# Optimization experiments

Hardware: AMD Instinct MI355X
Metric: run time of the kernel (lower is better)

Reference implementation:

```python
import jax, jax.numpy as jnp
import numpy as np

B, T, P, N, U, L, K = 32, 12, 12, 512, 64, 2, 2
C = 2 * U  # combined_dim = input_dim(rnn_units) + rnn_units = 128


def setup_inputs():
    ks = jax.random.split(jax.random.key(0), 24)
    inp = {
        'x': jax.random.normal(ks[0], (B, T, N, 1), jnp.float32),
        'adj': jax.random.uniform(ks[1], (N, N), jnp.float32),
        'spatial_mask_1': 0.1 * jax.random.normal(ks[2], (N, N), jnp.float32),
        'spatial_mask_2': 0.1 * jax.random.normal(ks[3], (N, N), jnp.float32),
        'temporal_mask': 0.1 * jax.random.normal(ks[4], (T, N), jnp.float32),
        'fc_in_w': 0.1 * jax.random.normal(ks[5], (1, U), jnp.float32),
        'fc_in_b': jnp.zeros((U,), jnp.float32),
        'fc_out_w': 0.1 * jax.random.normal(ks[6], (U, 1), jnp.float32),
        'fc_out_b': jnp.zeros((1,), jnp.float32),
    }
    i = 7
    for pre in ('enc', 'dec'):
        for name, od in (('w_ru', 2 * U), ('w_c', U), ('w_ru2', 2 * U), ('w_c2', U)):
            inp[pre + '_' + name] = 0.08 * jax.random.normal(ks[i], (L, 2 * K, C, od), jnp.float32)
            i += 1
            inp[pre + '_' + name.replace('w', 'b')] = jnp.zeros((L, od), jnp.float32)
    return inp


def _supports(adj):
    # adj_hat = A + I; fwd = D_out^-1 A_hat ; bwd = D_in^-1 A_hat^T (inf -> 0)
    ah = adj + jnp.eye(adj.shape[0], dtype=adj.dtype)
    d_out = ah.sum(1)
    d_in = ah.sum(0)
    inv_out = jnp.where(d_out > 0, 1.0 / d_out, 0.0)
    inv_in = jnp.where(d_in > 0, 1.0 / d_in, 0.0)
    return inv_out[:, None] * ah, inv_in[:, None] * ah.T


def _dgc(x, sup, w, b):
    # x: [B,N,C]; sup: (fwd,bwd) each [N,N]; w: [2K,C,O]; b: [O]
    # The torch code expands x K times per support, so each k-slice of x_out is
    # identical: sum_k P_s @ w[k] == P_s @ w[sK:(s+1)K].sum(0). Same math, fused.
    pf = jnp.einsum('nm,bni->bmi', sup[0], x)
    pb = jnp.einsum('nm,bni->bmi', sup[1], x)
    return (jnp.einsum('bni,io->bno', pf, w[:K].sum(0))
            + jnp.einsum('bni,io->bno', pb, w[K:].sum(0)) + b)


def _cell(x, h, s1, s2, w_ru, b_ru, w_c, b_c, w_ru2, b_ru2, w_c2, b_c2):
    xh = jnp.concatenate([x, h], axis=-1)
    r1, u1 = jnp.split(jax.nn.sigmoid(_dgc(xh, s1, w_ru, b_ru)), 2, axis=-1)
    c1 = jnp.tanh(_dgc(jnp.concatenate([x, r1 * h], axis=-1), s1, w_c, b_c))
    r2, u2 = jnp.split(jax.nn.sigmoid(_dgc(xh, s2, w_ru2, b_ru2)), 2, axis=-1)
    c2 = jnp.tanh(_dgc(jnp.concatenate([x, r2 * h], axis=-1), s2, w_c2, b_c2))
    u = 0.5 * (u1 + u2)
    c = 0.5 * (c1 + c2)
    return (1.0 - u) * h + u * c


def _forward(x, adj, sm1, sm2, tm, fc_in_w, fc_in_b, fc_out_w, fc_out_b, enc, dec):
    x = x * (jnp.tanh(tm) + 1.0)[None, :, :, None]
    adj1 = adj * (jnp.tanh(0.5 * (sm1 + sm1.T)) + 1.0)
    adj2 = adj * (jnp.tanh(0.5 * (sm2 + sm2.T)) + 1.0)
    s1 = _supports(adj1)
    s2 = _supports(adj2)

    def run_layers(cells, inp, h):
        hs = []
        for i in range(L):
            hi = _cell(inp, h[i], s1, s2, *[p[i] for p in cells])
            hs.append(hi)
            inp = hi
        return jnp.stack(hs)

    def enc_step(h, xt):
        inp = xt @ fc_in_w + fc_in_b  # [B,N,U]
        return run_layers(enc, inp, h), None

    h0 = jnp.zeros((L, B, N, U), x.dtype)
    h, _ = jax.lax.scan(enc_step, h0, jnp.swapaxes(x, 0, 1))

    def dec_step(carry, _):
        h, go = carry
        inp = go @ fc_in_w + fc_in_b
        h = run_layers(dec, inp, h)
        out_t = h[-1] @ fc_out_w + fc_out_b  # [B,N,1]
        return (h, out_t), out_t

    _, outs = jax.lax.scan(dec_step, (h, jnp.zeros((B, N, 1), x.dtype)), None, length=P)
    return jnp.swapaxes(outs, 0, 1)[..., 0]  # [B,P,N]


def reference(x, adj, spatial_mask_1, spatial_mask_2, temporal_mask,
              fc_in_w, fc_in_b, fc_out_w, fc_out_b,
              enc_w_ru, enc_b_ru, enc_w_c, enc_b_c, enc_w_ru2, enc_b_ru2, enc_w_c2, enc_b_c2,
              dec_w_ru, dec_b_ru, dec_w_c, dec_b_c, dec_w_ru2, dec_b_ru2, dec_w_c2, dec_b_c2):
    enc = (enc_w_ru, enc_b_ru, enc_w_c, enc_b_c, enc_w_ru2, enc_b_ru2, enc_w_c2, enc_b_c2)
    dec = (dec_w_ru, dec_b_ru, dec_w_c, dec_b_c, dec_w_ru2, dec_b_ru2, dec_w_c2, dec_b_c2)
    return _forward(x, adj, spatial_mask_1, spatial_mask_2, temporal_mask,
                    fc_in_w, fc_in_b, fc_out_w, fc_out_b, enc, dec)
```

## Files before the change

kernel.cpp:

```cpp
#include <hip/hip_runtime.h>
#include <math.h>

#define NN 512
#define BB 32
#define UU 64
#define CC 128
#define TT 12
#define NP 12
#define RRR (NN*BB)

typedef _Float16 f16;
typedef f16 f16x8 __attribute__((ext_vector_type(8)));
typedef f16 f16x4 __attribute__((ext_vector_type(4)));
typedef float f32x4 __attribute__((ext_vector_type(4)));

__device__ __forceinline__ void gload16(const f16* g, f16* l) {
  __builtin_amdgcn_global_load_lds((const __attribute__((address_space(1))) void*)g,
                                   (__attribute__((address_space(3))) void*)l, 16, 0, 0);
}

static const size_t OFF_ST    = 0;
static const size_t OFF_AH    = OFF_ST   + (size_t)4*512*512;
static const size_t OFF_INVD  = OFF_AH   + (size_t)2*512*512;
static const size_t OFF_XH    = OFF_INVD + 2048;
static const size_t OFF_H     = OFF_XH   + (size_t)2*RRR*CC;
static const size_t OFF_RH    = OFF_H    + (size_t)2*RRR*UU;
static const size_t OFF_U     = OFF_RH   + (size_t)2*RRR*UU;
static const size_t OFF_CB    = OFF_U    + (size_t)2*RRR*UU;
static const size_t OFF_F16   = OFF_CB   + (size_t)2*RRR*UU;
static const size_t OFF_ST16A = OFF_F16;
static const size_t OFF_ST16B = OFF_ST16A + 524288;
static const size_t OFF_XHT1  = OFF_ST16B + 524288;
static const size_t OFF_XHT2  = OFF_XHT1  + 1048576;
static const size_t OFF_RHT1  = OFF_XHT2  + 1048576;
static const size_t OFF_RHT2  = OFF_RHT1  + 1048576;
static const size_t OFF_P1    = OFF_RHT2  + 1048576;
static const size_t OFF_P2    = OFF_P1    + 4194304;
static const size_t OFF_Q1    = OFF_P2    + 4194304;
static const size_t OFF_Q2    = OFF_Q1    + 2097152;
static const size_t OFF_WT1   = OFF_Q2    + 2097152;
static const size_t OFF_WT2   = OFF_WT1   + 196608;

__global__ void k_build_ah(const float* __restrict__ adj, const float* __restrict__ sm1,
                           const float* __restrict__ sm2, float* __restrict__ ah) {
  int a = blockIdx.y, i = blockIdx.x;
  const float* sm = a ? sm2 : sm1;
  for (int j = threadIdx.x; j < NN; j += blockDim.x) {
    float m = tanhf(0.5f * (sm[i*NN + j] + sm[j*NN + i])) + 1.0f;
    ah[((size_t)a*NN + i)*NN + j] = adj[i*NN + j] * m + ((i == j) ? 1.0f : 0.0f);
  }
}

__global__ void k_deg(const float* __restrict__ ah, float* __restrict__ invd) {
  int a = blockIdx.y, n = blockIdx.x;
  const float* A = ah + (size_t)a*NN*NN;
  __shared__ float sr[256], sc[256];
  int t = threadIdx.x;
  sr[t] = A[(size_t)n*NN + t] + A[(size_t)n*NN + t + 256];
  sc[t] = A[(size_t)t*NN + n] + A[(size_t)(t+256)*NN + n];
  __syncthreads();
  for (int s = 128; s > 0; s >>= 1) {
    if (t < s) { sr[t] += sr[t+s]; sc[t] += sc[t+s]; }
    __syncthreads();
  }
  if (t == 0) {
    float dr = sr[0], dc = sc[0];
    invd[(a*2 + 0)*NN + n] = dr > 0.f ? 1.f/dr : 0.f;
    invd[(a*2 + 1)*NN + n] = dc > 0.f ? 1.f/dc : 0.f;
  }
}

__global__ void k_st(const float* __restrict__ ah, const float* __restrict__ invd,
                     float* __restrict__ ST) {
  int s = blockIdx.y, m = blockIdx.x;
  int a = s >> 1, dir = s & 1;
  const float* A = ah + (size_t)a*NN*NN;
  const float* inv = invd + (a*2 + dir)*NN;
  float* out = ST + ((size_t)s*NN + m)*NN;
  for (int n = threadIdx.x; n < NN; n += blockDim.x) {
    float v = dir ? A[(size_t)m*NN + n] : A[(size_t)n*NN + m];
    out[n] = inv[n] * v;
  }
}

__global__ void k_splitA(const float* __restrict__ s, f16* __restrict__ a1,
                         f16* __restrict__ a2, int total) {
  int i = blockIdx.x*blockDim.x + threadIdx.x;
  if (i >= total) return;
  float v = s[i] * 256.0f;
  f16 hi = (f16)v;
  a1[i] = hi;
  a2[i] = (f16)(v - (float)hi);
}

__global__ void k_wsumt(const float* __restrict__ w, f16* __restrict__ wt1,
                        f16* __restrict__ wt2, int O) {
  int idx = blockIdx.x*blockDim.x + threadIdx.x;
  int total = 2*2*O*128;
  if (idx >= total) return;
  int i  = idx & 127;
  int o  = (idx >> 7) % O;
  int fb = (idx / (128*O)) & 1;
  int l  = idx / (128*O*2);
  const float* wl = w + (((size_t)(l*4 + fb*2)*128 + i)*O + o);
  float v = (wl[0] + wl[(size_t)128*O]) * 256.0f;
  f16 hi = (f16)v;
  size_t dst = ((size_t)(l*2 + fb)*O + o)*128 + i;
  wt1[dst] = hi;
  wt2[dst] = (f16)(v - (float)hi);
}

__launch_bounds__(256)
__global__ void k_tsplit(const float* __restrict__ src, int lds_, long long srcZ,
                         f16* __restrict__ d1, f16* __restrict__ d2, long long dstZ) {
  __shared__ float tile[64][65];
  const float* S = src + (size_t)blockIdx.z*srcZ;
  f16* D1 = d1 + (size_t)blockIdx.z*dstZ;
  f16* D2 = d2 + (size_t)blockIdx.z*dstZ;
  int t = threadIdx.x;
  int c0 = blockIdx.x*64, k0 = blockIdx.y*64;
#pragma unroll
  for (int it = 0; it < 4; ++it) {
    int r = (t >> 4) + it*16;
    int c = (t & 15)*4;
    float4 v = *(const float4*)(S + (size_t)(k0 + r)*lds_ + c0 + c);
    tile[r][c] = v.x; tile[r][c+1] = v.y; tile[r][c+2] = v.z; tile[r][c+3] = v.w;
  }
  __syncthreads();
#pragma unroll
  for (int it = 0; it < 4; ++it) {
    int c = (t >> 4) + it*16;
    int ks = (t & 15)*4;
    f16x4 h1, h2;
#pragma unroll
    for (int j = 0; j < 4; ++j) {
      float v = tile[ks + j][c];
      f16 hi = (f16)v;
      h1[j] = hi;
      h2[j] = (f16)(v - (float)hi);
    }
    *(f16x4*)(D1 + (size_t)(c0 + c)*512 + k0 + ks) = h1;
    *(f16x4*)(D2 + (size_t)(c0 + c)*512 + k0 + ks) = h2;
  }
}

template<int MODE>
__launch_bounds__(256)
__global__ void k_mm16f(const f16* __restrict__ A1g, const f16* __restrict__ A2g, long long aZ,
                        const f16* __restrict__ B1g, const f16* __restrict__ B2g, long long bZ,
                        f16* __restrict__ C1g, f16* __restrict__ C2g, int ldc, long long cZ,
                        float scale) {
  const int bid = blockIdx.x;
  const int c = bid & 7, i = bid >> 3;
  int x, y; long long z;
  if (MODE == 0) { x = 2*c + (i & 1); y = i >> 1; z = 0; }
  else           { z = c >> 2; x = 2*(c & 3) + (i & 1); y = i >> 1; }
  const f16* A1 = A1g + z*aZ; const f16* A2 = A2g + z*aZ;
  const f16* B1 = B1g + z*bZ; const f16* B2 = B2g + z*bZ;
  f16* C1 = C1g + z*cZ; f16* C2 = C2g + z*cZ;
  const int row0 = x*128, col0 = y*128;

  __shared__ __align__(16) f16 As1[128*64], As2[128*64], Bs1[128*64], Bs2[128*64];
  const int tid = threadIdx.x;
  const int lane = tid & 63, w = tid >> 6;
  const int wr = w >> 1, wc = w & 1;
  const int rq = lane >> 3;
  const int gq = ((lane & 7) ^ rq) * 8;

  f32x4 acc[4][4];
#pragma unroll
  for (int m = 0; m < 4; ++m)
#pragma unroll
    for (int n = 0; n < 4; ++n) acc[m][n] = (f32x4){0.f,0.f,0.f,0.f};

  for (int k0 = 0; k0 < 512; k0 += 64) {
    __syncthreads();
#pragma unroll
    for (int q = 0; q < 4; ++q) {
      const int rloc = w*32 + q*8;
      gload16(A1 + (size_t)(row0 + rloc + rq)*512 + k0 + gq, As1 + rloc*64);
      gload16(A2 + (size_t)(row0 + rloc + rq)*512 + k0 + gq, As2 + rloc*64);
      gload16(B1 + (size_t)(col0 + rloc + rq)*512 + k0 + gq, Bs1 + rloc*64);
      gload16(B2 + (size_t)(col0 + rloc + rq)*512 + k0 + gq, Bs2 + rloc*64);
    }
    __syncthreads();
#pragma unroll
    for (int ks = 0; ks < 2; ++ks) {
      const int gk = ks*4 + (lane >> 4);
      f16x8 a1f[4], a2f[4], b1f[4], b2f[4];
#pragma unroll
      for (int m = 0; m < 4; ++m) {
        const int ra = wr*64 + m*16 + (lane & 15);
        const int sa = ra*64 + ((gk ^ (ra & 7))*8);
        a1f[m] = *(const f16x8*)(As1 + sa);
        a2f[m] = *(const f16x8*)(As2 + sa);
        const int rb = wc*64 + m*16 + (lane & 15);
        const int sb = rb*64 + ((gk ^ (rb & 7))*8);
        b1f[m] = *(const f16x8*)(Bs1 + sb);
        b2f[m] = *(const f16x8*)(Bs2 + sb);
      }
#pragma unroll
      for (int m = 0; m < 4; ++m)
#pragma unroll
        for (int n = 0; n < 4; ++n) {
          acc[m][n] = __builtin_amdgcn_mfma_f32_16x16x32_f16(a1f[m], b1f[n], acc[m][n], 0, 0, 0);
          acc[m][n] = __builtin_amdgcn_mfma_f32_16x16x32_f16(a1f[m], b2f[n], acc[m][n], 0, 0, 0);
          acc[m][n] = __builtin_amdgcn_mfma_f32_16x16x32_f16(a2f[m], b1f[n], acc[m][n], 0, 0, 0);
        }
    }
  }
#pragma unroll
  for (int m = 0; m < 4; ++m) {
    const int row = row0 + wr*64 + m*16 + (lane >> 4)*4;
#pragma unroll
    for (int n = 0; n < 4; ++n) {
      const int col = col0 + wc*64 + n*16 + (lane & 15);
#pragma unroll
      for (int r = 0; r < 4; ++r) {
        float v = acc[m][n][r] * scale;
        f16 hi = (f16)v;
        C1[(size_t)(row + r)*ldc + col] = hi;
        C2[(size_t)(row + r)*ldc + col] = (f16)(v - (float)hi);
      }
    }
  }
}

__launch_bounds__(256)
__global__ void k_gatesmf(const f16* __restrict__ P1, const f16* __restrict__ P2,
                          const f16* __restrict__ W1g0, const f16* __restrict__ W2g0,
                          const f16* __restrict__ W1g1, const f16* __restrict__ W2g1,
                          const float* __restrict__ b0, const float* __restrict__ b1,
                          const float* __restrict__ h,
                          float* __restrict__ rh, float* __restrict__ ubuf) {
  const int g = blockIdx.z;
  const f16* W1 = g ? W1g1 : W1g0;
  const f16* W2 = g ? W2g1 : W2g0;
  const float* bias = g ? b1 : b0;
  float* rh_g = rh   + (size_t)g * RRR * UU;
  float* u_g  = ubuf + (size_t)g * RRR * UU;
  __shared__ __align__(16) f16 As1[128*64], As2[128*64], Bs1[128*64], Bs2[128*64];
  const int tid = threadIdx.x;
  const int lane = tid & 63, w = tid >> 6;
  const int wr = w >> 1, wc = w & 1;
  const int R0 = blockIdx.x * 128;
  const int rq = lane >> 3;
  const int gq = ((lane & 7) ^ rq) * 8;

  f32x4 acc[4][4];
#pragma unroll
  for (int m = 0; m < 4; ++m)
#pragma unroll
    for (int n = 0; n < 4; ++n) acc[m][n] = (f32x4){0.f,0.f,0.f,0.f};

  for (int sup = 0; sup < 2; ++sup) {
    const f16* A1 = P1 + (size_t)(2*g + sup)*RRR*CC;
    const f16* A2 = P2 + (size_t)(2*g + sup)*RRR*CC;
    const f16* B1 = W1 + (size_t)sup*16384;
    const f16* B2 = W2 + (size_t)sup*16384;
    for (int k0 = 0; k0 < 128; k0 += 64) {
      __syncthreads();
#pragma unroll
      for (int q = 0; q < 4; ++q) {
        const int rloc = w*32 + q*8;
        gload16(A1 + (size_t)(R0 + rloc + rq)*128 + k0 + gq, As1 + rloc*64);
        gload16(A2 + (size_t)(R0 + rloc + rq)*128 + k0 + gq, As2 + rloc*64);
        gload16(B1 + (size_t)(rloc + rq)*128 + k0 + gq, Bs1 + rloc*64);
        gload16(B2 + (size_t)(rloc + rq)*128 + k0 + gq, Bs2 + rloc*64);
      }
      __syncthreads();
#pragma unroll
      for (int ks = 0; ks < 2; ++ks) {
        const int gk = ks*4 + (lane >> 4);
        f16x8 a1f[4], a2f[4], b1f[4], b2f[4];
#pragma unroll
        for (int m = 0; m < 4; ++m) {
          const int ra = wr*64 + m*16 + (lane & 15);
          const int sa = ra*64 + ((gk ^ (ra & 7))*8);
          a1f[m] = *(const f16x8*)(As1 + sa);
          a2f[m] = *(const f16x8*)(As2 + sa);
          const int rb = wc*64 + m*16 + (lane & 15);
          const int sb = rb*64 + ((gk ^ (rb & 7))*8);
          b1f[m] = *(const f16x8*)(Bs1 + sb);
          b2f[m] = *(const f16x8*)(Bs2 + sb);
        }
#pragma unroll
        for (int m = 0; m < 4; ++m)
#pragma unroll
          for (int n = 0; n < 4; ++n) {
            acc[m][n] = __builtin_amdgcn_mfma_f32_16x16x32_f16(a1f[m], b1f[n], acc[m][n], 0, 0, 0);
            acc[m][n] = __builtin_amdgcn_mfma_f32_16x16x32_f16(a1f[m], b2f[n], acc[m][n], 0, 0, 0);
            acc[m][n] = __builtin_amdgcn_mfma_f32_16x16x32_f16(a2f[m], b1f[n], acc[m][n], 0, 0, 0);
          }
      }
    }
  }
#pragma unroll
  for (int m = 0; m < 4; ++m) {
    const int row = R0 + wr*64 + m*16 + (lane >> 4)*4;
#pragma unroll
    for (int n = 0; n < 4; ++n) {
      const int o = wc*64 + n*16 + (lane & 15);
#pragma unroll
      for (int r = 0; r < 4; ++r) {
        const int R = row + r;
        float v = acc[m][n][r] * 0.00390625f + bias[o];
        float sg = 1.f / (1.f + expf(-v));
        if (o < 64) rh_g[(size_t)R*UU + o] = sg * h[(size_t)R*UU + o];
        else        u_g[(size_t)R*UU + o - 64] = sg;
      }
    }
  }
}

__launch_bounds__(256)
__global__ void k_candmf(const f16* __restrict__ P1, const f16* __restrict__ P2,
                         const f16* __restrict__ Q1, const f16* __restrict__ Q2,
                         const f16* __restrict__ Wc1g0, const f16* __restrict__ Wc2g0,
                         const f16* __restrict__ Wc1g1, const f16* __restrict__ Wc2g1,
                         const float* __restrict__ b0, const float* __restrict__ b1,
                         float* __restrict__ cbuf) {
  const int g = blockIdx.z;
  const f16* W1 = g ? Wc1g1 : Wc1g0;
  const f16* W2 = g ? Wc2g1 : Wc2g0;
  const float* bias = g ? b1 : b0;
  float* c_g = cbuf + (size_t)g * RRR * UU;
  __shared__ __align__(16) f16 As1[128*64], As2[128*64], Bs1[64*64], Bs2[64*64];
  const int tid = threadIdx.x;
  const int lane = tid & 63, w = tid >> 6;
  const int R0 = blockIdx.x * 128;
  const int rq = lane >> 3;
  const int gq = ((lane & 7) ^ rq) * 8;

  f32x4 acc[2][4];
#pragma unroll
  for (int m = 0; m < 2; ++m)
#pragma unroll
    for (int n = 0; n < 4; ++n) acc[m][n] = (f32x4){0.f,0.f,0.f,0.f};

  for (int seg = 0; seg < 4; ++seg) {
    const int sup = seg >> 1, isQ = seg & 1;
    const f16* A1 = isQ ? (Q1 + ((size_t)g*2 + sup)*1048576)
                        : (P1 + (size_t)(2*g + sup)*RRR*CC);
    const f16* A2 = isQ ? (Q2 + ((size_t)g*2 + sup)*1048576)
                        : (P2 + (size_t)(2*g + sup)*RRR*CC);
    const int lda = isQ ? 64 : 128;
    const f16* B1 = W1 + (size_t)sup*8192 + (isQ ? 64 : 0);
    const f16* B2 = W2 + (size_t)sup*8192 + (isQ ? 64 : 0);
    __syncthreads();
#pragma unroll
    for (int q = 0; q < 4; ++q) {
      const int rloc = w*32 + q*8;
      gload16(A1 + (size_t)(R0 + rloc + rq)*lda + gq, As1 + rloc*64);
      gload16(A2 + (size_t)(R0 + rloc + rq)*lda + gq, As2 + rloc*64);
    }
#pragma unroll
    for (int q = 0; q < 2; ++q) {
      const int rloc = w*16 + q*8;
      gload16(B1 + (size_t)(rloc + rq)*128 + gq, Bs1 + rloc*64);
      gload16(B2 + (size_t)(rloc + rq)*128 + gq, Bs2 + rloc*64);
    }
    __syncthreads();
#pragma unroll
    for (int ks = 0; ks < 2; ++ks) {
      const int gk = ks*4 + (lane >> 4);
      f16x8 a1f[2], a2f[2], b1f[4], b2f[4];
#pragma unroll
      for (int m = 0; m < 2; ++m) {
        const int ra = w*32 + m*16 + (lane & 15);
        const int sa = ra*64 + ((gk ^ (ra & 7))*8);
        a1f[m] = *(const f16x8*)(As1 + sa);
        a2f[m] = *(const f16x8*)(As2 + sa);
      }
#pragma unroll
      for (int n = 0; n < 4; ++n) {
        const int rb = n*16 + (lane & 15);
        const int sb = rb*64 + ((gk ^ (rb & 7))*8);
        b1f[n] = *(const f16x8*)(Bs1 + sb);
        b2f[n] = *(const f16x8*)(Bs2 + sb);
      }
#pragma unroll
      for (int m = 0; m < 2; ++m)
#pragma unroll
        for (int n = 0; n < 4; ++n) {
          acc[m][n] = __builtin_amdgcn_mfma_f32_16x16x32_f16(a1f[m], b1f[n], acc[m][n], 0, 0, 0);
          acc[m][n] = __builtin_amdgcn_mfma_f32_16x16x32_f16(a1f[m], b2f[n], acc[m][n], 0, 0, 0);
          acc[m][n] = __builtin_amdgcn_mfma_f32_16x16x32_f16(a2f[m], b1f[n], acc[m][n], 0, 0, 0);
        }
    }
  }
#pragma unroll
  for (int m = 0; m < 2; ++m) {
    const int row = R0 + w*32 + m*16 + (lane >> 4)*4;
#pragma unroll
    for (int n = 0; n < 4; ++n) {
      const int o = n*16 + (lane & 15);
#pragma unroll
      for (int r = 0; r < 4; ++r)
        c_g[(size_t)(row + r)*UU + o] = tanhf(acc[m][n][r] * 0.00390625f + bias[o]);
    }
  }
}

__global__ void k_xin(const float* __restrict__ x, const float* __restrict__ tm,
                      const float* __restrict__ fiw, const float* __restrict__ fib,
                      float* __restrict__ xh0, int t) {
  int idx = blockIdx.x*blockDim.x + threadIdx.x;
  int u = idx & 63, R = idx >> 6;
  int b = R & 31, n = R >> 5;
  float xs = x[((size_t)b*TT + t)*NN + n] * (tanhf(tm[t*NN + n]) + 1.0f);
  xh0[(size_t)R*CC + u] = xs * fiw[u] + fib[u];
}

__global__ void k_decin0(const float* __restrict__ fib, float* __restrict__ xh0) {
  int idx = blockIdx.x*blockDim.x + threadIdx.x;
  int u = idx & 63, R = idx >> 6;
  xh0[(size_t)R*CC + u] = fib[u];
}

__global__ void k_update(const float* __restrict__ u1, const float* __restrict__ u2,
                         const float* __restrict__ c1, const float* __restrict__ c2,
                         float* __restrict__ h, float* __restrict__ xh,
                         float* __restrict__ xh_next) {
  int idx = blockIdx.x*blockDim.x + threadIdx.x;
  int R = idx >> 6, o = idx & 63;
  float u = 0.5f*(u1[idx] + u2[idx]);
  float c = 0.5f*(c1[idx] + c2[idx]);
  float hn = (1.f - u)*h[idx] + u*c;
  h[idx] = hn;
  xh[(size_t)R*CC + 64 + o] = hn;
  if (xh_next) xh_next[(size_t)R*CC + o] = hn;
}

__global__ void k_out(const float* __restrict__ h1, const float* __restrict__ fow,
                      const float* __restrict__ fob, const float* __restrict__ fiw,
                      const float* __restrict__ fib, float* __restrict__ out,
                      float* __restrict__ xh0, int p) {
  int R = blockIdx.x*blockDim.x + threadIdx.x;
  int b = R & 31, n = R >> 5;
  const float* hr = h1 + (size_t)R*UU;
  float s = fob[0];
#pragma unroll
  for (int u = 0; u < UU; ++u) s = fmaf(hr[u], fow[u], s);
  out[(size_t)b*(NP*NN) + (size_t)p*NN + n] = s;
#pragma unroll
  for (int u = 0; u < UU; ++u) xh0[(size_t)R*CC + u] = fmaf(s, fiw[u], fib[u]);
}

extern "C" void kernel_launch(void* const* d_in, const int* in_sizes, int n_in,
                              void* d_out, int out_size, void* d_ws, size_t ws_size,
                              hipStream_t stream) {
  (void)in_sizes; (void)n_in; (void)out_size; (void)ws_size;
  const float* x   = (const float*)d_in[0];
  const float* adj = (const float*)d_in[1];
  const float* sm1 = (const float*)d_in[2];
  const float* sm2 = (const float*)d_in[3];
  const float* tm  = (const float*)d_in[4];
  const float* fiw = (const float*)d_in[5];
  const float* fib = (const float*)d_in[6];
  const float* fow = (const float*)d_in[7];
  const float* fob = (const float*)d_in[8];

  float* WS   = (float*)d_ws;
  float* ST   = WS + OFF_ST;
  float* AH   = WS + OFF_AH;
  float* INVD = WS + OFF_INVD;
  float* XH   = WS + OFF_XH;
  float* H    = WS + OFF_H;
  float* RH   = WS + OFF_RH;
  float* Ubuf = WS + OFF_U;
  float* Cbuf = WS + OFF_CB;
  f16* ST1  = (f16*)(WS + OFF_ST16A);
  f16* ST2  = (f16*)(WS + OFF_ST16B);
  f16* XHT1 = (f16*)(WS + OFF_XHT1);
  f16* XHT2 = (f16*)(WS + OFF_XHT2);
  f16* RHT1 = (f16*)(WS + OFF_RHT1);
  f16* RHT2 = (f16*)(WS + OFF_RHT2);
  f16* P1   = (f16*)(WS + OFF_P1);
  f16* P2   = (f16*)(WS + OFF_P2);
  f16* Q1   = (f16*)(WS + OFF_Q1);
  f16* Q2   = (f16*)(WS + OFF_Q2);
  f16* WT1  = (f16*)(WS + OFF_WT1);
  f16* WT2  = (f16*)(WS + OFF_WT2);

  k_build_ah<<<dim3(512,2),256,0,stream>>>(adj, sm1, sm2, AH);
  k_deg<<<dim3(512,2),256,0,stream>>>(AH, INVD);
  k_st<<<dim3(512,4),256,0,stream>>>(AH, INVD, ST);
  k_splitA<<<4096,256,0,stream>>>(ST, ST1, ST2, 2048*512);

  const int widx[8] = {9, 11, 13, 15, 17, 19, 21, 23};
  const int Osz[8]  = {128, 64, 128, 64, 128, 64, 128, 64};
  const size_t woff16[8] = {0, 65536, 98304, 163840, 196608, 262144, 294912, 360448};
  for (int tau = 0; tau < 8; ++tau) {
    int total = 2*2*Osz[tau]*128;
    k_wsumt<<<(total + 255)/256, 256, 0, stream>>>((const float*)d_in[widx[tau]],
                                                   WT1 + woff16[tau], WT2 + woff16[tau],
                                                   Osz[tau]);
  }

  hipMemsetAsync(XH, 0, (size_t)2*RRR*CC*sizeof(float), stream);
  hipMemsetAsync(H,  0, (size_t)2*RRR*UU*sizeof(float), stream);

  const float inv256 = 1.0f/256.0f;

  for (int step = 0; step < TT + NP; ++step) {
    const bool enc = step < TT;
    const int ph = enc ? 0 : 1;
    if (enc)             k_xin<<<4096,256,0,stream>>>(x, tm, fiw, fib, XH, step);
    else if (step == TT) k_decin0<<<4096,256,0,stream>>>(fib, XH);

    for (int l = 0; l < 2; ++l) {
      float* xh_l = XH + (size_t)l*RRR*CC;
      float* h_l  = H  + (size_t)l*RRR*UU;
      const size_t lru = (size_t)l*2*128*128;
      const size_t lc  = (size_t)l*2*64*128;
      const f16* Wru1a = WT1 + woff16[ph*4+0] + lru;
      const f16* Wru2a = WT2 + woff16[ph*4+0] + lru;
      const f16* Wru1b = WT1 + woff16[ph*4+2] + lru;
      const f16* Wru2b = WT2 + woff16[ph*4+2] + lru;
      const f16* Wc1a  = WT1 + woff16[ph*4+1] + lc;
      const f16* Wc2a  = WT2 + woff16[ph*4+1] + lc;
      const f16* Wc1b  = WT1 + woff16[ph*4+3] + lc;
      const f16* Wc2b  = WT2 + woff16[ph*4+3] + lc;
      const float* bru  = (const float*)d_in[enc?10:18] + (size_t)l*128;
      const float* bc   = (const float*)d_in[enc?12:20] + (size_t)l*64;
      const float* bru2 = (const float*)d_in[enc?14:22] + (size_t)l*128;
      const float* bc2  = (const float*)d_in[enc?16:24] + (size_t)l*64;

      k_tsplit<<<dim3(64,8,1),256,0,stream>>>(xh_l, 4096, 0, XHT1, XHT2, 0);
      k_mm16f<0><<<512,256,0,stream>>>(ST1, ST2, 0, XHT1, XHT2, 0,
                                       P1, P2, 4096, 0, inv256);
      k_gatesmf<<<dim3(128,1,2),256,0,stream>>>(P1, P2, Wru1a, Wru2a, Wru1b, Wru2b,
                                                bru, bru2, h_l, RH, Ubuf);
      k_tsplit<<<dim3(32,8,2),256,0,stream>>>(RH, 2048, (long long)RRR*UU,
                                              RHT1, RHT2, (long long)2048*512);
      k_mm16f<1><<<256,256,0,stream>>>(ST1, ST2, (long long)1024*512,
                                       RHT1, RHT2, (long long)2048*512,
                                       Q1, Q2, 2048, (long long)1024*2048, inv256);
      k_candmf<<<dim3(128,1,2),256,0,stream>>>(P1, P2, Q1, Q2, Wc1a, Wc2a, Wc1b, Wc2b,
                                               bc, bc2, Cbuf);
      k_update<<<4096,256,0,stream>>>(Ubuf, Ubuf + (size_t)RRR*UU,
                                      Cbuf, Cbuf + (size_t)RRR*UU,
                                      h_l, xh_l, (l == 0) ? (XH + (size_t)RRR*CC) : nullptr);
    }
    if (!enc) {
      int p = step - TT;
      k_out<<<64,256,0,stream>>>(H + (size_t)RRR*UU, fow, fob, fiw, fib,
                                 (float*)d_out, XH, p);
    }
  }
}
```

Measured before the change: 5.354 ms.

## Exploit rank-1 input projection for layer-0 diffusion and fuse candidate with update

Layer 0's input half of xh is an affine function of a scalar per node (x·w_in + b_in). Its graph diffusion is therefore computed as S·sx and rowsum(S) in fp32, then expanded, instead of being run through the full 128-column f16x2 split GEMM. The layer-0 GEMM now only covers the 64 hidden columns and writes them into the upper half of P. Separately, the candidate kernel now handles both gate groups in one block and applies the GRU update directly, which removes the Cbuf round trip and the separate k_update launch. Trade-offs: the new kernel has fewer blocks (128) and higher register use, and several small kernels are added.

```diff
diff --git a/kernel.cpp b/kernel.cpp
--- a/kernel.cpp
+++ b/kernel.cpp
@@ -27,6 +27,9 @@
 static const size_t OFF_RH    = OFF_H    + (size_t)2*RRR*UU;
 static const size_t OFF_U     = OFF_RH   + (size_t)2*RRR*UU;
 static const size_t OFF_CB    = OFF_U    + (size_t)2*RRR*UU;
+static const size_t OFF_SX    = OFF_CB;
+static const size_t OFF_PS    = OFF_SX   + 16384;
+static const size_t OFF_SROW  = OFF_PS   + 65536;
 static const size_t OFF_F16   = OFF_CB   + (size_t)2*RRR*UU;
 static const size_t OFF_ST16A = OFF_F16;
 static const size_t OFF_ST16B = OFF_ST16A + 524288;
@@ -81,6 +84,19 @@
     float v = dir ? A[(size_t)m*NN + n] : A[(size_t)n*NN + m];
     out[n] = inv[n] * v;
   }
+}
+
+__global__ void k_srow(const float* __restrict__ ST, float* __restrict__ SRow) {
+  int row = blockIdx.x;
+  int t = threadIdx.x;
+  __shared__ float red[256];
+  red[t] = ST[(size_t)row*512 + t] + ST[(size_t)row*512 + t + 256];
+  __syncthreads();
+  for (int s = 128; s > 0; s >>= 1) {
+    if (t < s) red[t] += red[t+s];
+    __syncthreads();
+  }
+  if (t == 0) SRow[row] = red[0];
 }
 
 __global__ void k_splitA(const float* __restrict__ s, f16* __restrict__ a1,
@@ -110,6 +126,59 @@
   wt2[dst] = (f16)(v - (float)hi);
 }
 
+__global__ void k_sx(const float* __restrict__ x, const float* __restrict__ tm,
+                     float* __restrict__ SX, int t) {
+  int R = blockIdx.x*blockDim.x + threadIdx.x;
+  int b = R & 31, n = R >> 5;
+  SX[R] = x[((size_t)b*TT + t)*NN + n] * (tanhf(tm[t*NN + n]) + 1.0f);
+}
+
+__launch_bounds__(256)
+__global__ void k_ps(const float* __restrict__ ST, const float* __restrict__ SX,
+                     float* __restrict__ PS) {
+  int row = blockIdx.x;
+  int t = threadIdx.x;
+  int b = t & 31, g = t >> 5;
+  const float* Sr = ST + (size_t)row*512 + g*64;
+  const float* Sx = SX + (size_t)g*64*32 + b;
+  float p = 0.f;
+#pragma unroll
+  for (int k = 0; k < 64; ++k) p = fmaf(Sr[k], Sx[(size_t)k*32], p);
+  __shared__ float red[8][32];
+  red[g][b] = p;
+  __syncthreads();
+  if (g == 0) {
+    float s = 0.f;
+#pragma unroll
+    for (int q = 0; q < 8; ++q) s += red[q][b];
+    PS[(size_t)row*32 + b] = s;
+  }
+}
+
+__global__ void k_pxfill(const float* __restrict__ PS, const float* __restrict__ SRow,
+                         const float* __restrict__ fiw, const float* __restrict__ fib,
+                         f16* __restrict__ P1, f16* __restrict__ P2) {
+  int idx = blockIdx.x*blockDim.x + threadIdx.x;
+  int u8 = idx & 7;
+  int R = (idx >> 3) & 16383;
+  int sup = idx >> 17;
+  int m = R >> 5, b = R & 31;
+  float ps = PS[((size_t)sup*512 + m)*32 + b];
+  float sr = SRow[(size_t)sup*512 + m];
+  f16x8 h1, h2;
+#pragma unroll
+  for (int j = 0; j < 8; ++j) {
+    int u = u8*8 + j;
+    float v = ps*fiw[u] + sr*fib[u];
+    f16 hi = (f16)v;
+    h1[j] = hi;
+    h2[j] = (f16)(v - (float)hi);
+  }
+  size_t dst = (size_t)sup*RRR*CC + (size_t)R*CC + u8*8;
+  *(f16x8*)(P1 + dst) = h1;
+  *(f16x8*)(P2 + dst) = h2;
+}
+
 __launch_bounds__(256)
 __global__ void k_tsplit(const float* __restrict__ src, int lds_, long long srcZ,
                          f16* __restrict__ d1, f16* __restrict__ d2, long long dstZ) {
@@ -153,8 +222,9 @@
   const int bid = blockIdx.x;
   const int c = bid & 7, i = bid >> 3;
   int x, y; long long z;
-  if (MODE == 0) { x = 2*c + (i & 1); y = i >> 1; z = 0; }
-  else           { z = c >> 2; x = 2*(c & 3) + (i & 1); y = i >> 1; }
+  if (MODE == 0)      { x = 2*c + (i & 1); y = i >> 1; z = 0; }
+  else if (MODE == 1) { z = c >> 2; x = 2*(c & 3) + (i & 1); y = i >> 1; }
+  else                { x = 2*c + (i & 1); y = i >> 1; z = 0; }
   const f16* A1 = A1g + z*aZ; const f16* A2 = A2g + z*aZ;
   const f16* B1 = B1g + z*bZ; const f16* B2 = B2g + z*bZ;
   f16* C1 = C1g + z*cZ; f16* C2 = C2g + z*cZ;
@@ -214,7 +284,10 @@
     const int row = row0 + wr*64 + m*16 + (lane >> 4)*4;
 #pragma unroll
     for (int n = 0; n < 4; ++n) {
-      const int col = col0 + wc*64 + n*16 + (lane & 15);
+      const int rest = n*16 + (lane & 15);
+      int col;
+      if (MODE == 2) col = col0*2 + wc*128 + 64 + rest;
+      else           col = col0 + wc*64 + rest;
 #pragma unroll
       for (int r = 0; r < 4; ++r) {
         float v = acc[m][n][r] * scale;
@@ -314,17 +387,14 @@
 }
 
 __launch_bounds__(256)
-__global__ void k_candmf(const f16* __restrict__ P1, const f16* __restrict__ P2,
-                         const f16* __restrict__ Q1, const f16* __restrict__ Q2,
-                         const f16* __restrict__ Wc1g0, const f16* __restrict__ Wc2g0,
-                         const f16* __restrict__ Wc1g1, const f16* __restrict__ Wc2g1,
-                         const float* __restrict__ b0, const float* __restrict__ b1,
-                         float* __restrict__ cbuf) {
-  const int g = blockIdx.z;
-  const f16* W1 = g ? Wc1g1 : Wc1g0;
-  const f16* W2 = g ? Wc2g1 : Wc2g0;
-  const float* bias = g ? b1 : b0;
-  float* c_g = cbuf + (size_t)g * RRR * UU;
+__global__ void k_candupd(const f16* __restrict__ P1, const f16* __restrict__ P2,
+                          const f16* __restrict__ Q1, const f16* __restrict__ Q2,
+                          const f16* __restrict__ Wc1g0, const f16* __restrict__ Wc2g0,
+                          const f16* __restrict__ Wc1g1, const f16* __restrict__ Wc2g1,
+                          const float* __restrict__ b0, const float* __restrict__ b1,
+                          const float* __restrict__ ubuf,
+                          float* __restrict__ h, float* __restrict__ xh_self,
+                          float* __restrict__ xh_next) {
   __shared__ __align__(16) f16 As1[128*64], As2[128*64], Bs1[64*64], Bs2[64*64];
   const int tid = threadIdx.x;
   const int lane = tid & 63, w = tid >> 6;
@@ -332,110 +402,94 @@
   const int rq = lane >> 3;
   const int gq = ((lane & 7) ^ rq) * 8;
 
-  f32x4 acc[2][4];
-#pragma unroll
-  for (int m = 0; m < 2; ++m)
-#pragma unroll
-    for (int n = 0; n < 4; ++n) acc[m][n] = (f32x4){0.f,0.f,0.f,0.f};
-
-  for (int seg = 0; seg < 4; ++seg) {
-    const int sup = seg >> 1, isQ = seg & 1;
-    const f16* A1 = isQ ? (Q1 + ((size_t)g*2 + sup)*1048576)
-                        : (P1 + (size_t)(2*g + sup)*RRR*CC);
-    const f16* A2 = isQ ? (Q2 + ((size_t)g*2 + sup)*1048576)
-                        : (P2 + (size_t)(2*g + sup)*RRR*CC);
-    const int lda = isQ ? 64 : 128;
-    const f16* B1 = W1 + (size_t)sup*8192 + (isQ ? 64 : 0);
-    const f16* B2 = W2 + (size_t)sup*8192 + (isQ ? 64 : 0);
-    __syncthreads();
-#pragma unroll
-    for (int q = 0; q < 4; ++q) {
-      const int rloc = w*32 + q*8;
-      gload16(A1 + (size_t)(R0 + rloc + rq)*lda + gq, As1 + rloc*64);
-      gload16(A2 + (size_t)(R0 + rloc + rq)*lda + gq, As2 + rloc*64);
-    }
-#pragma unroll
-    for (int q = 0; q < 2; ++q) {
-      const int rloc = w*16 + q*8;
-      gload16(B1 + (size_t)(rloc + rq)*128 + gq, Bs1 + rloc*64);
-      gload16(B2 + (size_t)(rloc + rq)*128 + gq, Bs2 + rloc*64);
-    }
-    __syncthreads();
-#pragma unroll
-    for (int ks = 0; ks < 2; ++ks) {
-      const int gk = ks*4 + (lane >> 4);
-      f16x8 a1f[2], a2f[2], b1f[4], b2f[4];
-#pragma unroll
-      for (int m = 0; m < 2; ++m) {
-        const int ra = w*32 + m*16 + (lane & 15);
-        const int sa = ra*64 + ((gk ^ (ra & 7))*8);
-        a1f[m] = *(const f16x8*)(As1 + sa);
-        a2f[m] = *(const f16x8*)(As2 + sa);
-      }
-#pragma unroll
-      for (int n = 0; n < 4; ++n) {
-        const int rb = n*16 + (lane & 15);
-        const int sb = rb*64 + ((gk ^ (rb & 7))*8);
-        b1f[n] = *(const f16x8*)(Bs1 + sb);
-        b2f[n] = *(const f16x8*)(Bs2 + sb);
-      }
-#pragma unroll
-      for (int m = 0; m < 2; ++m)
+  f32x4 acc[2][2][4];
+#pragma unroll
+  for (int g = 0; g < 2; ++g)
+#pragma unroll
+    for (int m = 0; m < 2; ++m)
+#pragma unroll
+      for (int n = 0; n < 4; ++n) acc[g][m][n] = (f32x4){0.f,0.f,0.f,0.f};
+
+  for (int g = 0; g < 2; ++g) {
+    const f16* W1 = g ? Wc1g1 : Wc1g0;
+    const f16* W2 = g ? Wc2g1 : Wc2g0;
+    for (int seg = 0; seg < 4; ++seg) {
+      const int sup = seg >> 1, isQ = seg & 1;
+      const f16* A1 = isQ ? (Q1 + ((size_t)g*2 + sup)*1048576)
+                          : (P1 + (size_t)(2*g + sup)*RRR*CC);
+      const f16* A2 = isQ ? (Q2 + ((size_t)g*2 + sup)*1048576)
+                          : (P2 + (size_t)(2*g + sup)*RRR*CC);
+      const int lda = isQ ? 64 : 128;
+      const f16* B1 = W1 + (size_t)sup*8192 + (isQ ? 64 : 0);
+      const f16* B2 = W2 + (size_t)sup*8192 + (isQ ? 64 : 0);
+      __syncthreads();
+#pragma unroll
+      for (int q = 0; q < 4; ++q) {
+        const int rloc = w*32 + q*8;
+        gload16(A1 + (size_t)(R0 + rloc + rq)*lda + gq, As1 + rloc*64);
+        gload16(A2 + (size_t)(R0 + rloc + rq)*lda + gq, As2 + rloc*64);
+      }
+#pragma unroll
+      for (int q = 0; q < 2; ++q) {
+        const int rloc = w*16 + q*8;
+        gload16(B1 + (size_t)(rloc + rq)*128 + gq, Bs1 + rloc*64);
+        gload16(B2 + (size_t)(rloc + rq)*128 + gq, Bs2 + rloc*64);
+      }
+      __syncthreads();
+#pragma unroll
+      for (int ks = 0; ks < 2; ++ks) {
+        const int gk = ks*4 + (lane >> 4);
+        f16x8 a1f[2], a2f[2], b1f[4], b2f[4];
+#pragma unroll
+        for (int m = 0; m < 2; ++m) {
+          const int ra = w*32 + m*16 + (lane & 15);
+          const int sa = ra*64 + ((gk ^ (ra & 7))*8);
+          a1f[m] = *(const f16x8*)(As1 + sa);
+          a2f[m] = *(const f16x8*)(As2 + sa);
+        }
 #pragma unroll
         for (int n = 0; n < 4; ++n) {
-          acc[m][n] = __builtin_amdgcn_mfma_f32_16x16x32_f16(a1f[m], b1f[n], acc[m][n], 0, 0, 0);
-          acc[m][n] = __builtin_amdgcn_mfma_f32_16x16x32_f16(a1f[m], b2f[n], acc[m][n], 0, 0, 0);
-          acc[m][n] = __builtin_amdgcn_mfma_f32_16x16x32_f16(a2f[m], b1f[n], acc[m][n], 0, 0, 0);
+          const int rb = n*16 + (lane & 15);
+          const int sb = rb*64 + ((gk ^ (rb & 7))*8);
+          b1f[n] = *(const f16x8*)(Bs1 + sb);
+          b2f[n] = *(const f16x8*)(Bs2 + sb);
         }
+#pragma unroll
+        for (int m = 0; m < 2; ++m)
+#pragma unroll
+          for (int n = 0; n < 4; ++n) {
+            acc[g][m][n] = __builtin_amdgcn_mfma_f32_16x16x32_f16(a1f[m], b1f[n], acc[g][m][n], 0, 0, 0);
+            acc[g][m][n] = __builtin_amdgcn_mfma_f32_16x16x32_f16(a1f[m], b2f[n], acc[g][m][n], 0, 0, 0);
+            acc[g][m][n] = __builtin_amdgcn_mfma_f32_16x16x32_f16(a2f[m], b1f[n], acc[g][m][n], 0, 0, 0);
+          }
+      }
     }
   }
 #pragma unroll
   for (int m = 0; m < 2; ++m) {
-    const int row = R0 + w*32 + m*16 + (lane >> 4)*4;
 #pragma unroll
     for (int n = 0; n < 4; ++n) {
       const int o = n*16 + (lane & 15);
 #pragma unroll
-      for (int r = 0; r < 4; ++r)
-        c_g[(size_t)(row + r)*UU + o] = tanhf(acc[m][n][r] * 0.00390625f + bias[o]);
-    }
-  }
-}
-
-__global__ void k_xin(const float* __restrict__ x, const float* __restrict__ tm,
-                      const float* __restrict__ fiw, const float* __restrict__ fib,
-                      float* __restrict__ xh0, int t) {
-  int idx = blockIdx.x*blockDim.x + threadIdx.x;
-  int u = idx & 63, R = idx >> 6;
-  int b = R & 31, n = R >> 5;
-  float xs = x[((size_t)b*TT + t)*NN + n] * (tanhf(tm[t*NN + n]) + 1.0f);
-  xh0[(size_t)R*CC + u] = xs * fiw[u] + fib[u];
-}
-
-__global__ void k_decin0(const float* __restrict__ fib, float* __restrict__ xh0) {
-  int idx = blockIdx.x*blockDim.x + threadIdx.x;
-  int u = idx & 63, R = idx >> 6;
-  xh0[(size_t)R*CC + u] = fib[u];
-}
-
-__global__ void k_update(const float* __restrict__ u1, const float* __restrict__ u2,
-                         const float* __restrict__ c1, const float* __restrict__ c2,
-                         float* __restrict__ h, float* __restrict__ xh,
-                         float* __restrict__ xh_next) {
-  int idx = blockIdx.x*blockDim.x + threadIdx.x;
-  int R = idx >> 6, o = idx & 63;
-  float u = 0.5f*(u1[idx] + u2[idx]);
-  float c = 0.5f*(c1[idx] + c2[idx]);
-  float hn = (1.f - u)*h[idx] + u*c;
-  h[idx] = hn;
-  xh[(size_t)R*CC + 64 + o] = hn;
-  if (xh_next) xh_next[(size_t)R*CC + o] = hn;
+      for (int r = 0; r < 4; ++r) {
+        const int R = R0 + w*32 + m*16 + (lane >> 4)*4 + r;
+        const size_t idx = (size_t)R*UU + o;
+        float c1 = tanhf(acc[0][m][n][r] * 0.00390625f + b0[o]);
+        float c2 = tanhf(acc[1][m][n][r] * 0.00390625f + b1[o]);
+        float u = 0.5f*(ubuf[idx] + ubuf[(size_t)RRR*UU + idx]);
+        float cc = 0.5f*(c1 + c2);
+        float hn = (1.f - u)*h[idx] + u*cc;
+        h[idx] = hn;
+        if (xh_self) xh_self[(size_t)R*CC + 64 + o] = hn;
+        if (xh_next) xh_next[(size_t)R*CC + o] = hn;
+      }
+    }
+  }
 }
 
 __global__ void k_out(const float* __restrict__ h1, const float* __restrict__ fow,
-                      const float* __restrict__ fob, const float* __restrict__ fiw,
-                      const float* __restrict__ fib, float* __restrict__ out,
-                      float* __restrict__ xh0, int p) {
+                      const float* __restrict__ fob, float* __restrict__ out,
+                      float* __restrict__ SX, int p) {
   int R = blockIdx.x*blockDim.x + threadIdx.x;
   int b = R & 31, n = R >> 5;
   const float* hr = h1 + (size_t)R*UU;
@@ -443,8 +497,7 @@
 #pragma unroll
   for (int u = 0; u < UU; ++u) s = fmaf(hr[u], fow[u], s);
   out[(size_t)b*(NP*NN) + (size_t)p*NN + n] = s;
-#pragma unroll
-  for (int u = 0; u < UU; ++u) xh0[(size_t)R*CC + u] = fmaf(s, fiw[u], fib[u]);
+  SX[R] = s;
 }
 
 extern "C" void kernel_launch(void* const* d_in, const int* in_sizes, int n_in,
@@ -469,7 +522,9 @@
   float* H    = WS + OFF_H;
   float* RH   = WS + OFF_RH;
   float* Ubuf = WS + OFF_U;
-  float* Cbuf = WS + OFF_CB;
+  float* SX   = WS + OFF_SX;
+  float* PS   = WS + OFF_PS;
+  float* SRow = WS + OFF_SROW;
   f16* ST1  = (f16*)(WS + OFF_ST16A);
   f16* ST2  = (f16*)(WS + OFF_ST16B);
   f16* XHT1 = (f16*)(WS + OFF_XHT1);
@@ -487,6 +542,7 @@
   k_deg<<<dim3(512,2),256,0,stream>>>(AH, INVD);
   k_st<<<dim3(512,4),256,0,stream>>>(AH, INVD, ST);
   k_splitA<<<4096,256,0,stream>>>(ST, ST1, ST2, 2048*512);
+  k_srow<<<2048,256,0,stream>>>(ST, SRow);
 
   const int widx[8] = {9, 11, 13, 15, 17, 19, 21, 23};
   const int Osz[8]  = {128, 64, 128, 64, 128, 64, 128, 64};
@@ -506,11 +562,13 @@
   for (int step = 0; step < TT + NP; ++step) {
     const bool enc = step < TT;
     const int ph = enc ? 0 : 1;
-    if (enc)             k_xin<<<4096,256,0,stream>>>(x, tm, fiw, fib, XH, step);
-    else if (step == TT) k_decin0<<<4096,256,0,stream>>>(fib, XH);
+    if (enc)             k_sx<<<64,256,0,stream>>>(x, tm, SX, step);
+    else if (step == TT) hipMemsetAsync(SX, 0, 16384*sizeof(float), stream);
+
+    k_ps<<<2048,256,0,stream>>>(ST, SX, PS);
 
     for (int l = 0; l < 2; ++l) {
-      float* xh_l = XH + (size_t)l*RRR*CC;
+      float* xh1  = XH + (size_t)RRR*CC;
       float* h_l  = H  + (size_t)l*RRR*UU;
       const size_t lru = (size_t)l*2*128*128;
       const size_t lc  = (size_t)l*2*64*128;
@@ -527,9 +585,16 @@
       const float* bru2 = (const float*)d_in[enc?14:22] + (size_t)l*128;
       const float* bc2  = (const float*)d_in[enc?16:24] + (size_t)l*64;
 
-      k_tsplit<<<dim3(64,8,1),256,0,stream>>>(xh_l, 4096, 0, XHT1, XHT2, 0);
-      k_mm16f<0><<<512,256,0,stream>>>(ST1, ST2, 0, XHT1, XHT2, 0,
-                                       P1, P2, 4096, 0, inv256);
+      if (l == 0) {
+        k_tsplit<<<dim3(32,8,1),256,0,stream>>>(h_l, 2048, 0, XHT1, XHT2, 0);
+        k_mm16f<2><<<256,256,0,stream>>>(ST1, ST2, 0, XHT1, XHT2, 0,
+                                         P1, P2, 4096, 0, inv256);
+        k_pxfill<<<2048,256,0,stream>>>(PS, SRow, fiw, fib, P1, P2);
+      } else {
+        k_tsplit<<<dim3(64,8,1),256,0,stream>>>(xh1, 4096, 0, XHT1, XHT2, 0);
+        k_mm16f<0><<<512,256,0,stream>>>(ST1, ST2, 0, XHT1, XHT2, 0,
+                                         P1, P2, 4096, 0, inv256);
+      }
       k_gatesmf<<<dim3(128,1,2),256,0,stream>>>(P1, P2, Wru1a, Wru2a, Wru1b, Wru2b,
                                                 bru, bru2, h_l, RH, Ubuf);
       k_tsplit<<<dim3(32,8,2),256,0,stream>>>(RH, 2048, (long long)RRR*UU,
@@ -537,16 +602,15 @@
       k_mm16f<1><<<256,256,0,stream>>>(ST1, ST2, (long long)1024*512,
                                        RHT1, RHT2, (long long)2048*512,
                                        Q1, Q2, 2048, (long long)1024*2048, inv256);
-      k_candmf<<<dim3(128,1,2),256,0,stream>>>(P1, P2, Q1, Q2, Wc1a, Wc2a, Wc1b, Wc2b,
-                                               bc, bc2, Cbuf);
-      k_update<<<4096,256,0,stream>>>(Ubuf, Ubuf + (size_t)RRR*UU,
-                                      Cbuf, Cbuf + (size_t)RRR*UU,
-                                      h_l, xh_l, (l == 0) ? (XH + (size_t)RRR*CC) : nullptr);
+      k_candupd<<<128,256,0,stream>>>(P1, P2, Q1, Q2, Wc1a, Wc2a, Wc1b, Wc2b,
+                                      bc, bc2, Ubuf, h_l,
+                                      (l == 1) ? xh1 : nullptr,
+                                      (l == 0) ? xh1 : nullptr);
     }
     if (!enc) {
       int p = step - TT;
-      k_out<<<64,256,0,stream>>>(H + (size_t)RRR*UU, fow, fob, fiw, fib,
-                                 (float*)d_out, XH, p);
-    }
-  }
-}
+      k_out<<<64,256,0,stream>>>(H + (size_t)RRR*UU, fow, fob,
+                                 (float*)d_out, SX, p);
+    }
+  }
+}
```

Result: slower. 5.799 ms (+8.3%).
